# Kernel tuning notes

Measured on AMD Instinct MI355X. Metric: run time of the kernel, lower is better.

## Reference

```python
import jax, jax.numpy as jnp
import numpy as np

M, R, ITERS = 262144, 64, 3


def setup_inputs() -> dict:
    key = jax.random.key(0)
    x = jax.random.normal(key, (M, R, 2), dtype=jnp.float32)
    return {"x": x}


def _gram_schmidt(x):
    # x: (M, R, 2) real -> complex (M, R)
    xc = x[..., 0] + 1j * x[..., 1]
    m, r = xc.shape

    def outer(Q, i):
        # Modified Gram-Schmidt for column i. Columns j >= i of Q are still
        # exactly zero, so scanning over ALL columns subtracts coeff=0 for
        # j >= i and is bit-identical to the original j < i loop.
        q0 = jnp.take(xc, i, axis=1)  # (M,)

        def inner(q, qj):
            coeff = jnp.sum(jnp.conj(qj) * q)
            return q - coeff * qj, None

        q, _ = jax.lax.scan(inner, q0, jnp.swapaxes(Q, 0, 1))
        norm = jnp.sqrt(jnp.sum(jnp.abs(q) ** 2) + 1e-10)
        Q = jax.lax.dynamic_update_slice(Q, (q / norm)[:, None], (0, i))
        return Q, None

    Q, _ = jax.lax.scan(outer, jnp.zeros_like(xc), jnp.arange(r))

    # Iterative QR refinement (Bjorck-style correction, damping 0.4)
    I = jnp.eye(r, dtype=Q.dtype)
    for _ in range(ITERS):
        gram = jnp.conj(Q.T) @ Q                      # (R, R)
        Q = Q - Q @ ((gram - I) * 0.4)                # (M, R)
        norms = jnp.sqrt(jnp.sum(jnp.abs(Q) ** 2, axis=0, keepdims=True) + 1e-10)
        Q = Q / norms

    return jnp.stack([Q.real, Q.imag], axis=-1)      # (M, R, 2)


def reference(x):
    return _gram_schmidt(x)
```

## Files before the change

kernel.cpp:

```cpp
#include <hip/hip_runtime.h>
#include <math.h>

#define NCOL 64
#define M_ROWS 262144

typedef short bf16x8 __attribute__((ext_vector_type(8)));
typedef float f32x4 __attribute__((ext_vector_type(4)));
typedef unsigned int u32x4 __attribute__((ext_vector_type(4)));

__device__ __forceinline__ unsigned short f2bf(float f) {
    unsigned int u = __float_as_uint(f);
    u += 0x7FFFu + ((u >> 16) & 1u);
    return (unsigned short)(u >> 16);
}
__device__ __forceinline__ float bf2f(unsigned short s) {
    return __uint_as_float(((unsigned int)s) << 16);
}
__device__ __forceinline__ unsigned int bfrnd(float f) {
    unsigned int u = __float_as_uint(f);
    return u + 0x7FFFu + ((u >> 16) & 1u);
}
__device__ __forceinline__ unsigned int perm_hi16(unsigned int lo, unsigned int hi) {
    return __builtin_amdgcn_perm(hi, lo, 0x07060302u);
}
__device__ __forceinline__ bf16x8 as_bf16x8(u32x4 v) { return __builtin_bit_cast(bf16x8, v); }

#define GR_BLOCKS 512
#define GR_KTILES (M_ROWS / 32 / GR_BLOCKS)

__device__ __forceinline__ void stage_gram(const float4* __restrict__ src4,
                                           float4* lds0, int t) {
#pragma unroll
    for (int i = 0; i < 4; ++i) {
        const int f = t + 256 * i;
        const int sf = f ^ (((f >> 8) & 1) << 2);
        const int base = __builtin_amdgcn_readfirstlane(f & ~63);
        __builtin_amdgcn_global_load_lds(
            (const __attribute__((address_space(1))) unsigned int*)(src4 + sf),
            (__attribute__((address_space(3))) unsigned int*)(lds0 + base), 16, 0, 0);
    }
}

__global__ __launch_bounds__(256) void gram_mfma(const float* __restrict__ X,
                                                 float* __restrict__ Sbufs) {
    __shared__ float4 buf[3][1024];
    const int t = threadIdx.x;
    const int w = t >> 6, l = t & 63, r = l & 15, c = l >> 4;

    f32x4 acc[2][8];
#pragma unroll
    for (int jr = 0; jr < 2; ++jr)
#pragma unroll
        for (int kt = 0; kt < 8; ++kt) acc[jr][kt] = (f32x4){0.f, 0.f, 0.f, 0.f};

    const float4* Xt4 = reinterpret_cast<const float4*>(X) + (size_t)blockIdx.x * 512 * 32;
    const int rb = c * 4096 + r * 4;
    const int cx = (c & 1);

    stage_gram(Xt4, &buf[0][0], t);
    stage_gram(Xt4 + 1024, &buf[1][0], t);

    for (int tt = 0; tt < GR_KTILES; ++tt) {
        if (tt + 2 < GR_KTILES) {
            stage_gram(Xt4 + (size_t)(tt + 2) * 1024, &buf[(tt + 2) % 3][0], t);
            asm volatile("s_waitcnt vmcnt(8)" ::: "memory");
        } else if (tt + 1 < GR_KTILES) {
            asm volatile("s_waitcnt vmcnt(4)" ::: "memory");
        } else {
            asm volatile("s_waitcnt vmcnt(0)" ::: "memory");
        }
        __builtin_amdgcn_sched_barrier(0);
        __builtin_amdgcn_s_barrier();
        __builtin_amdgcn_sched_barrier(0);

        const char* bb = (const char*)&buf[tt % 3][0];
        bf16x8 frag[8];
#pragma unroll
        for (int kt = 0; kt < 8; ++kt) {
            const int cb = (kt ^ cx) * 64;
            float x[8];
#pragma unroll
            for (int i = 0; i < 8; ++i)
                x[i] = *(const float*)(bb + rb + i * 512 + cb);
            u32x4 pw;
#pragma unroll
            for (int wd = 0; wd < 4; ++wd)
                pw[wd] = perm_hi16(bfrnd(x[2 * wd]), bfrnd(x[2 * wd + 1]));
            frag[kt] = as_bf16x8(pw);
        }
#pragma unroll
        for (int s = 0; s < 8; ++s) {
            if ((s >> 1) == w) {
#pragma unroll
                for (int kt = 0; kt < 8; ++kt)
                    acc[s & 1][kt] = __builtin_amdgcn_mfma_f32_16x16x32_bf16(
                        frag[s], frag[kt], acc[s & 1][kt], 0, 0, 0);
            }
        }
        __builtin_amdgcn_s_barrier();
    }

    float* lds = reinterpret_cast<float*>(&buf[0][0]);
    float4* Sb4 = reinterpret_cast<float4*>(Sbufs + (size_t)blockIdx.x * 16384);
#pragma unroll
    for (int jr = 0; jr < 2; ++jr) {
#pragma unroll
        for (int kt = 0; kt < 8; ++kt)
#pragma unroll
            for (int q = 0; q < 4; ++q)
                lds[(w * 16 + 4 * c + q) * 128 + 16 * kt + r] = acc[jr][kt][q];
        __syncthreads();
#pragma unroll
        for (int s2 = 0; s2 < 8; ++s2) {
            const int f = t + 256 * s2;
            const int row = f >> 5;
            const int gr = 32 * (row >> 4) + 16 * jr + (row & 15);
            Sb4[gr * 32 + (f & 31)] = reinterpret_cast<const float4*>(lds)[f];
        }
        __syncthreads();
    }
}

__global__ __launch_bounds__(256) void reduce_s(const float4* __restrict__ Sbufs,
                                                float4* __restrict__ Sfinal) {
    __shared__ float4 part[256];
    const int t = threadIdx.x;
    const int slot = blockIdx.x * 16 + (t & 15);
    const int bg = t >> 4;
    float4 s = (float4){0.f, 0.f, 0.f, 0.f};
    for (int b = bg * 32; b < bg * 32 + 32; ++b) {
        const float4 u = Sbufs[(size_t)b * 4096 + slot];
        s.x += u.x; s.y += u.y; s.z += u.z; s.w += u.w;
    }
    part[t] = s;
    __syncthreads();
    for (int off = 128; off >= 16; off >>= 1) {
        if (t < off) {
            float4 a = part[t], b2 = part[t + off];
            a.x += b2.x; a.y += b2.y; a.z += b2.z; a.w += b2.w;
            part[t] = a;
        }
        __syncthreads();
    }
    if (t < 16) Sfinal[slot] = part[t];
}

__global__ __launch_bounds__(256) void make_w(const float* __restrict__ S,
                                              unsigned int* __restrict__ W2h,
                                              unsigned int* __restrict__ W2l) {
    __shared__ float2 A1s[64 * 64];
    __shared__ float2 Wc[64 * 16];
    __shared__ float dinv[64];
    const int t = threadIdx.x;
    const int cb = blockIdx.x * 16;

    if (t < 64)
        dinv[t] = rsqrtf(fmaxf(S[(2 * t) * 128 + 2 * t] + S[(2 * t + 1) * 128 + 2 * t + 1],
                               1e-30f));
    __syncthreads();

    for (int e = t; e < 4096; e += 256) {
        const int j = e >> 6, k = e & 63;
        float2 v = make_float2(0.f, 0.f);
        if (j < k) {
            const float s00 = S[(2 * j) * 128 + 2 * k];
            const float s01 = S[(2 * j) * 128 + 2 * k + 1];
            const float s10 = S[(2 * j + 1) * 128 + 2 * k];
            const float s11 = S[(2 * j + 1) * 128 + 2 * k + 1];
            const float sc = dinv[j] * dinv[k];
            v = make_float2((s00 + s11) * sc, (s01 - s10) * sc);
        }
        A1s[e] = v;
    }
    __syncthreads();

    const int c = cb + (t & 15);
    const int j0 = (t >> 4) * 4;
    float2 m1[4], sq[4];
#pragma unroll
    for (int q = 0; q < 4; ++q) { m1[q] = make_float2(0.f, 0.f); sq[q] = make_float2(0.f, 0.f); }
    for (int m = 0; m < 64; ++m) {
        const float2 amc = A1s[m * 64 + c];
#pragma unroll
        for (int q = 0; q < 4; ++q) {
            const int j = j0 + q;
            const float2 amj = A1s[m * 64 + j];
            const float2 ajm = A1s[j * 64 + m];
            m1[q].x = fmaf(amj.x, amc.x, fmaf(amj.y, amc.y, m1[q].x));
            m1[q].y = fmaf(amj.x, amc.y, fmaf(-amj.y, amc.x, m1[q].y));
            sq[q].x = fmaf(ajm.x, amc.x, fmaf(-ajm.y, amc.y, sq[q].x));
            sq[q].y = fmaf(ajm.x, amc.y, fmaf( ajm.y, amc.x, sq[q].y));
        }
    }

#pragma unroll
    for (int q = 0; q < 4; ++q) {
        const int j = j0 + q;
        float2 v;
        if (j < c) {
            const float2 a = A1s[j * 64 + c];
            v = make_float2(-a.x + m1[q].x + sq[q].x, -a.y + m1[q].y + sq[q].y);
        } else if (j == c) {
            v = make_float2(1.f + 0.5f * m1[q].x, 0.f);
        } else {
            v = make_float2(0.f, 0.f);
        }
        const float dj = dinv[j];
        Wc[j * 16 + (t & 15)] = make_float2(v.x * dj, v.y * dj);
    }
    __syncthreads();

    for (int e = t; e < 2048; e += 256) {
        const int row = 2 * cb + (e >> 6);
        const int j = e & 63;
        const int k = row >> 1;
        const float2 v = (j <= k) ? Wc[j * 16 + (k - cb)] : make_float2(0.f, 0.f);
        float lo, hi;
        if (row & 1) { lo = v.y; hi = v.x; }
        else         { lo = v.x; hi = -v.y; }
        const unsigned short lo_h = f2bf(lo);
        const unsigned short lo_l = f2bf(lo - bf2f(lo_h));
        const unsigned short hi_h = f2bf(hi);
        const unsigned short hi_l = f2bf(hi - bf2f(hi_h));
        W2h[row * 64 + j] = (unsigned int)lo_h | ((unsigned int)hi_h << 16);
        W2l[row * 64 + j] = (unsigned int)lo_l | ((unsigned int)hi_l << 16);
    }
}

#define AP_BLOCKS 2048
#define AP_RTILES 8

__device__ __forceinline__ void stage_tile(const float4* __restrict__ src4,
                                           float4* lds0, int t) {
#pragma unroll
    for (int i = 0; i < 2; ++i) {
        const int f = t + 256 * i;
        const int sf = f ^ ((f >> 5) & 7);
        const int base = __builtin_amdgcn_readfirstlane(f & ~63);
        __builtin_amdgcn_global_load_lds(
            (const __attribute__((address_space(1))) unsigned int*)(src4 + sf),
            (__attribute__((address_space(3))) unsigned int*)(lds0 + base), 16, 0, 0);
    }
}

__global__ __launch_bounds__(256) void apply_mfma(const float* __restrict__ X,
                                                  const unsigned short* __restrict__ W2h,
                                                  const unsigned short* __restrict__ W2l,
                                                  float* __restrict__ Q) {
    __shared__ float4 buf[2][512];
    const int t = threadIdx.x;
    const int w = t >> 6, l = t & 63, r = l & 15, c = l >> 4;

    bf16x8 bh[2][4], bl[2][4];
#pragma unroll
    for (int ct = 0; ct < 2; ++ct)
#pragma unroll
        for (int kc = 0; kc < 4; ++kc) {
            const int idx = (32 * w + 16 * ct + r) * 128 + kc * 32 + c * 8;
            bh[ct][kc] = *reinterpret_cast<const bf16x8*>(W2h + idx);
            bl[ct][kc] = *reinterpret_cast<const bf16x8*>(W2l + idx);
        }
    __builtin_amdgcn_sched_barrier(0);

    const size_t m0 = (size_t)blockIdx.x * (AP_RTILES * 16);
    const float4* Xt = reinterpret_cast<const float4*>(X) + m0 * 32;
    float* qp = Q + (m0 + 4 * c) * 128 + 32 * w + r;
    const int swz = (r & 7) << 4;

    stage_tile(Xt, &buf[0][0], t);

#pragma unroll
    for (int tt = 0; tt < AP_RTILES; ++tt) {
        if (tt + 1 < AP_RTILES)
            stage_tile(Xt + (size_t)(tt + 1) * 512, &buf[(tt + 1) & 1][0], t);
        if (tt == 0)                     { asm volatile("s_waitcnt vmcnt(2)" ::: "memory"); }
        else if (tt == AP_RTILES - 1)    { asm volatile("s_waitcnt vmcnt(8)" ::: "memory"); }
        else                             { asm volatile("s_waitcnt vmcnt(10)" ::: "memory"); }
        __builtin_amdgcn_sched_barrier(0);
        __builtin_amdgcn_s_barrier();
        __builtin_amdgcn_sched_barrier(0);

        const char* bb = (const char*)&buf[tt & 1][0];
        bf16x8 ah[4];
#pragma unroll
        for (int kc = 0; kc < 4; ++kc) {
            const int base = r * 512 + kc * 128 + c * 32;
            const float4 v0 = *(const float4*)(bb + ((base) ^ swz));
            const float4 v1 = *(const float4*)(bb + ((base + 16) ^ swz));
            u32x4 hw;
            hw[0] = perm_hi16(bfrnd(v0.x), bfrnd(v0.y));
            hw[1] = perm_hi16(bfrnd(v0.z), bfrnd(v0.w));
            hw[2] = perm_hi16(bfrnd(v1.x), bfrnd(v1.y));
            hw[3] = perm_hi16(bfrnd(v1.z), bfrnd(v1.w));
            ah[kc] = as_bf16x8(hw);
        }
        f32x4 acc[2];
        acc[0] = (f32x4){0.f, 0.f, 0.f, 0.f};
        acc[1] = (f32x4){0.f, 0.f, 0.f, 0.f};
#pragma unroll
        for (int kc = 0; kc < 4; ++kc)
#pragma unroll
            for (int ct = 0; ct < 2; ++ct) {
                acc[ct] = __builtin_amdgcn_mfma_f32_16x16x32_bf16(ah[kc], bh[ct][kc], acc[ct], 0, 0, 0);
                acc[ct] = __builtin_amdgcn_mfma_f32_16x16x32_bf16(ah[kc], bl[ct][kc], acc[ct], 0, 0, 0);
            }
        float* qt = qp + (size_t)tt * 16 * 128;
#pragma unroll
        for (int ct = 0; ct < 2; ++ct)
#pragma unroll
            for (int q = 0; q < 4; ++q)
                qt[q * 128 + ct * 16] = acc[ct][q];
        __builtin_amdgcn_s_barrier();
    }
}

extern "C" void kernel_launch(void* const* d_in, const int* in_sizes, int n_in,
                              void* d_out, int out_size, void* d_ws, size_t ws_size,
                              hipStream_t stream) {
    (void)in_sizes; (void)n_in; (void)out_size; (void)ws_size;
    const float* X = reinterpret_cast<const float*>(d_in[0]);
    float* Q = reinterpret_cast<float*>(d_out);

    float* Sbufs = reinterpret_cast<float*>(d_ws);
    char* pextra = (char*)d_ws + (size_t)GR_BLOCKS * 65536;
    float* Sfinal = reinterpret_cast<float*>(pextra);
    unsigned int* W2h = reinterpret_cast<unsigned int*>(pextra + 65536);
    unsigned int* W2l = reinterpret_cast<unsigned int*>(pextra + 65536 + 32768);

    gram_mfma<<<GR_BLOCKS, 256, 0, stream>>>(X, Sbufs);
    reduce_s<<<256, 256, 0, stream>>>(reinterpret_cast<const float4*>(Sbufs),
                                      reinterpret_cast<float4*>(Sfinal));
    make_w<<<4, 256, 0, stream>>>(Sfinal, W2h, W2l);
    apply_mfma<<<AP_BLOCKS, 256, 0, stream>>>(X, reinterpret_cast<const unsigned short*>(W2h),
                                              reinterpret_cast<const unsigned short*>(W2l), Q);
}
```

Before: 104.0 us.

## Compact per-block Gram partials, triple-buffer apply staging, nontemporal Q stores

The gram kernel now writes only the upper-triangular block groups of each per-block partial Gram matrix into a compact layout. This cuts the workspace written by gram_mfma and read by reduce_s, and reduce_s scatters the reduced values back to the full layout with fewer blocks. The apply kernel moves from double to triple buffering of X tiles, prefetching two tiles ahead with retuned vmcnt waits. Output stores are now nontemporal to avoid cache pollution. The trade-off is more LDS, hand-tuned wait counts that must match the load counts, and the lower triangle of Sfinal is no longer written, so make_w must read only the upper part.

```diff
diff --git a/kernel.cpp b/kernel.cpp
--- a/kernel.cpp
+++ b/kernel.cpp
@@ -7,6 +7,9 @@
 typedef short bf16x8 __attribute__((ext_vector_type(8)));
 typedef float f32x4 __attribute__((ext_vector_type(4)));
 typedef unsigned int u32x4 __attribute__((ext_vector_type(4)));
+
+__device__ __constant__ const int OFF_G[8] = {0, 512, 960, 1344, 1664, 1920, 2112, 2240};
+#define S_COMPACT_F4 2304
 
 __device__ __forceinline__ unsigned short f2bf(float f) {
     unsigned int u = __float_as_uint(f);
@@ -101,7 +104,8 @@
     }
 
     float* lds = reinterpret_cast<float*>(&buf[0][0]);
-    float4* Sb4 = reinterpret_cast<float4*>(Sbufs + (size_t)blockIdx.x * 16384);
+    const float4* lds4 = reinterpret_cast<const float4*>(lds);
+    float4* Sb4 = reinterpret_cast<float4*>(Sbufs) + (size_t)blockIdx.x * S_COMPACT_F4;
 #pragma unroll
     for (int jr = 0; jr < 2; ++jr) {
 #pragma unroll
@@ -111,11 +115,15 @@
                 lds[(w * 16 + 4 * c + q) * 128 + 16 * kt + r] = acc[jr][kt][q];
         __syncthreads();
 #pragma unroll
-        for (int s2 = 0; s2 < 8; ++s2) {
-            const int f = t + 256 * s2;
-            const int row = f >> 5;
-            const int gr = 32 * (row >> 4) + 16 * jr + (row & 15);
-            Sb4[gr * 32 + (f & 31)] = reinterpret_cast<const float4*>(lds)[f];
+        for (int gi = 0; gi < 4; ++gi) {
+            const int g = 2 * gi + jr;
+            const int len = 32 - 4 * g;
+            const int cnt = 16 * len;
+            for (int s = t; s < cnt; s += 256) {
+                const int u = s / len;
+                const int cf = s - u * len;
+                Sb4[OFF_G[g] + s] = lds4[(gi * 16 + u) * 32 + 4 * g + cf];
+            }
         }
         __syncthreads();
     }
@@ -129,7 +137,7 @@
     const int bg = t >> 4;
     float4 s = (float4){0.f, 0.f, 0.f, 0.f};
     for (int b = bg * 32; b < bg * 32 + 32; ++b) {
-        const float4 u = Sbufs[(size_t)b * 4096 + slot];
+        const float4 u = Sbufs[(size_t)b * S_COMPACT_F4 + slot];
         s.x += u.x; s.y += u.y; s.z += u.z; s.w += u.w;
     }
     part[t] = s;
@@ -142,7 +150,20 @@
         }
         __syncthreads();
     }
-    if (t < 16) Sfinal[slot] = part[t];
+    if (t < 16) {
+        int g = 0;
+#pragma unroll
+        for (int h = 1; h < 8; ++h) if (slot >= OFF_G[h]) g = h;
+        int u = 0, cf = 0;
+#pragma unroll
+        for (int h = 0; h < 8; ++h)
+            if (g == h) {
+                const int rem = slot - OFF_G[h];
+                u = rem / (32 - 4 * h);
+                cf = rem - u * (32 - 4 * h);
+            }
+        Sfinal[(16 * g + u) * 32 + 4 * g + cf] = part[t];
+    }
 }
 
 __global__ __launch_bounds__(256) void make_w(const float* __restrict__ S,
@@ -247,7 +268,7 @@
                                                   const unsigned short* __restrict__ W2h,
                                                   const unsigned short* __restrict__ W2l,
                                                   float* __restrict__ Q) {
-    __shared__ float4 buf[2][512];
+    __shared__ float4 buf[3][512];
     const int t = threadIdx.x;
     const int w = t >> 6, l = t & 63, r = l & 15, c = l >> 4;
 
@@ -268,19 +289,22 @@
     const int swz = (r & 7) << 4;
 
     stage_tile(Xt, &buf[0][0], t);
+    stage_tile(Xt + 512, &buf[1][0], t);
 
 #pragma unroll
     for (int tt = 0; tt < AP_RTILES; ++tt) {
-        if (tt + 1 < AP_RTILES)
-            stage_tile(Xt + (size_t)(tt + 1) * 512, &buf[(tt + 1) & 1][0], t);
-        if (tt == 0)                     { asm volatile("s_waitcnt vmcnt(2)" ::: "memory"); }
-        else if (tt == AP_RTILES - 1)    { asm volatile("s_waitcnt vmcnt(8)" ::: "memory"); }
-        else                             { asm volatile("s_waitcnt vmcnt(10)" ::: "memory"); }
+        if (tt + 2 < AP_RTILES)
+            stage_tile(Xt + (size_t)(tt + 2) * 512, &buf[(tt + 2) % 3][0], t);
+        if (tt == 0)                     { asm volatile("s_waitcnt vmcnt(4)" ::: "memory"); }
+        else if (tt == 1)                { asm volatile("s_waitcnt vmcnt(12)" ::: "memory"); }
+        else if (tt == AP_RTILES - 2)    { asm volatile("s_waitcnt vmcnt(18)" ::: "memory"); }
+        else if (tt == AP_RTILES - 1)    { asm volatile("s_waitcnt vmcnt(16)" ::: "memory"); }
+        else                             { asm volatile("s_waitcnt vmcnt(20)" ::: "memory"); }
         __builtin_amdgcn_sched_barrier(0);
         __builtin_amdgcn_s_barrier();
         __builtin_amdgcn_sched_barrier(0);
 
-        const char* bb = (const char*)&buf[tt & 1][0];
+        const char* bb = (const char*)&buf[tt % 3][0];
         bf16x8 ah[4];
 #pragma unroll
         for (int kc = 0; kc < 4; ++kc) {
@@ -309,7 +333,7 @@
         for (int ct = 0; ct < 2; ++ct)
 #pragma unroll
             for (int q = 0; q < 4; ++q)
-                qt[q * 128 + ct * 16] = acc[ct][q];
+                __builtin_nontemporal_store(acc[ct][q], qt + q * 128 + ct * 16);
         __builtin_amdgcn_s_barrier();
     }
 }
@@ -322,13 +346,13 @@
     float* Q = reinterpret_cast<float*>(d_out);
 
     float* Sbufs = reinterpret_cast<float*>(d_ws);
-    char* pextra = (char*)d_ws + (size_t)GR_BLOCKS * 65536;
+    char* pextra = (char*)d_ws + (size_t)GR_BLOCKS * (S_COMPACT_F4 * 16);
     float* Sfinal = reinterpret_cast<float*>(pextra);
     unsigned int* W2h = reinterpret_cast<unsigned int*>(pextra + 65536);
     unsigned int* W2l = reinterpret_cast<unsigned int*>(pextra + 65536 + 32768);
 
     gram_mfma<<<GR_BLOCKS, 256, 0, stream>>>(X, Sbufs);
-    reduce_s<<<256, 256, 0, stream>>>(reinterpret_cast<const float4*>(Sbufs),
+    reduce_s<<<144, 256, 0, stream>>>(reinterpret_cast<const float4*>(Sbufs),
                                       reinterpret_cast<float4*>(Sfinal));
     make_w<<<4, 256, 0, stream>>>(Sfinal, W2h, W2l);
     apply_mfma<<<AP_BLOCKS, 256, 0, stream>>>(X, reinterpret_cast<const unsigned short*>(W2h),
```

After: 106.3 us. 1.02x slower.
